# Kernel optimization log

Hardware: AMD Instinct MI355X
Metric: run time of the kernel (lower is better)

Reference implementation:

```python
import jax, jax.numpy as jnp
import numpy as np

N = 50000      # nodes
E = 600000     # edges
IN = 128       # input_dim
HID = 128      # hidden_dim
OUT = 128      # output_dim
H = 4          # heads
D = OUT // H   # head dim
R = 4          # rel_num
L = 2          # n_layer
M = 10000      # len(idx)
EPS = 1e-5


def setup_inputs() -> dict:
    key = jax.random.key(0)
    ks = jax.random.split(key, 16)
    f = jax.random.normal
    inp = {
        "x": f(ks[0], (N, IN), jnp.float32),
        "proj_w": f(ks[1], (IN, HID), jnp.float32) / np.sqrt(IN).astype(np.float32),
        "proj_b": jnp.zeros((HID,), jnp.float32),
        "bn_gamma": jnp.ones((HID,), jnp.float32),
        "bn_beta": jnp.zeros((HID,), jnp.float32),
        # per-layer HGTConv params (stacked on leading L axis; layer0 in=HID, layer1 in=OUT, equal here)
        "q_w": f(ks[2], (L, HID, OUT), jnp.float32) / np.sqrt(HID).astype(np.float32),
        "q_b": jnp.zeros((L, OUT), jnp.float32),
        "k_w": f(ks[3], (L, HID, OUT), jnp.float32) / np.sqrt(HID).astype(np.float32),
        "k_b": jnp.zeros((L, OUT), jnp.float32),
        "v_w": f(ks[4], (L, HID, OUT), jnp.float32) / np.sqrt(HID).astype(np.float32),
        "v_b": jnp.zeros((L, OUT), jnp.float32),
        "a_w": f(ks[5], (L, OUT, OUT), jnp.float32) / np.sqrt(OUT).astype(np.float32),
        "a_b": jnp.zeros((L, OUT), jnp.float32),
        "skip": jnp.ones((L,), jnp.float32),
        "a_rel": f(ks[6], (L, R, H, D, D), jnp.float32) / np.sqrt(D).astype(np.float32),
        "m_rel": f(ks[7], (L, R, H, D, D), jnp.float32) / np.sqrt(D).astype(np.float32),
        "p_rel": jnp.ones((L, R, H), jnp.float32),
        "edge_index": jax.random.randint(ks[8], (2, E), 0, N, dtype=jnp.int32),
        "edge_type": jax.random.randint(ks[9], (E,), 0, R, dtype=jnp.int32),
        "idx": jax.random.randint(ks[10], (M,), 0, N, dtype=jnp.int32),
    }
    return inp


def _hgt_forward(x, proj_w, proj_b, bn_gamma, bn_beta, q_w, q_b, k_w, k_b, v_w, v_b,
                 a_w, a_b, skip, a_rel, m_rel, p_rel, edge_index, edge_type, idx):
    # proj + BatchNorm1d (training-mode batch statistics, biased variance)
    h = x @ proj_w + proj_b
    mu = h.mean(axis=0)
    var = jnp.mean((h - mu) ** 2, axis=0)
    h = (h - mu) * jax.lax.rsqrt(var + EPS) * bn_gamma + bn_beta

    src, dst = edge_index[0], edge_index[1]          # message from src(j) to dst(i)
    seg = dst * R + edge_type                        # per-(dst, relation) softmax segments
    scale = np.float32(1.0 / np.sqrt(D))

    for l in range(L):
        q = (h @ q_w[l] + q_b[l]).reshape(N, H, D)
        k = (h @ k_w[l] + k_b[l]).reshape(N, H, D)
        v = (h @ v_w[l] + v_b[l]).reshape(N, H, D)
        # relation-specific key/value transforms for every node/relation: [N,R,H,D]
        k_all = jnp.einsum('nhd,rhde->nrhe', k, a_rel[l])
        v_all = jnp.einsum('nhd,rhde->nrhe', v, m_rel[l])
        k_e = k_all[src, edge_type]                  # [E,H,D]
        v_e = v_all[src, edge_type]                  # [E,H,D]
        score = jnp.sum(q[dst] * k_e, axis=-1) * p_rel[l][edge_type] * scale  # [E,H]
        # per-relation segment softmax over incoming edges of each dst node
        smax = jax.ops.segment_max(score, seg, num_segments=N * R)
        e = jnp.exp(score - smax[seg])
        denom = jax.ops.segment_sum(e, seg, num_segments=N * R)
        alpha = e / denom[seg]                        # [E,H]
        out = jax.ops.segment_sum(alpha[..., None] * v_e, dst, num_segments=N)
        out = out.reshape(N, OUT)
        out = jax.nn.gelu(out, approximate=False) @ a_w[l] + a_b[l]
        b = jax.nn.sigmoid(skip[l])                   # learned skip gate
        h = b * out + (1.0 - b) * h                   # dims match -> residual mix
    return h[idx]


def reference(x, proj_w, proj_b, bn_gamma, bn_beta, q_w, q_b, k_w, k_b, v_w, v_b,
              a_w, a_b, skip, a_rel, m_rel, p_rel, edge_index, edge_type, idx):
    return _hgt_forward(x, proj_w, proj_b, bn_gamma, bn_beta, q_w, q_b, k_w, k_b,
                        v_w, v_b, a_w, a_b, skip, a_rel, m_rel, p_rel,
                        edge_index, edge_type, idx)
```

## Files before the change

### kernel.cpp

```cpp
#include <hip/hip_runtime.h>
#include <math.h>

#define NN 50000
#define EE 600000
#define MOUT 10000
#define DEGCAP 384
#define NT4 (NN * 4)

typedef short bf16x8 __attribute__((ext_vector_type(8)));
typedef float f32x4 __attribute__((ext_vector_type(4)));

__device__ __forceinline__ unsigned short f2bf(float x) {
    unsigned int u = __float_as_uint(x);
    u = (u + 0x7FFFu + ((u >> 16) & 1u)) >> 16;
    return (unsigned short)u;
}
__device__ __forceinline__ float bf2f(unsigned int b) {
    return __uint_as_float(b << 16);
}

__global__ __launch_bounds__(256) void prep_kernel(
    const float* __restrict__ proj_w, const float* __restrict__ a_w,
    const float* __restrict__ q_w, const float* __restrict__ q_b,
    const float* __restrict__ a_rel,
    const float* __restrict__ k_w, const float* __restrict__ k_b,
    const float* __restrict__ v_w, const float* __restrict__ v_b,
    const float* __restrict__ m_rel, const float* __restrict__ p_rel,
    const float* __restrict__ x,
    unsigned short* __restrict__ wt_pa, unsigned short* __restrict__ qkvw,
    float* __restrict__ fbias, unsigned short* __restrict__ msg_wt,
    unsigned short* __restrict__ x_bf, int* __restrict__ cnt,
    float* __restrict__ stats)
{
    const int b = blockIdx.x, t = threadIdx.x;
    if (b < 192) {
        int wi = b >> 6;
        int flat = (b & 63) * 256 + t;
        int n = flat >> 7, c = flat & 127;
        const float* src = (wi == 0) ? proj_w : (wi == 1) ? a_w : a_w + 16384;
        wt_pa[(size_t)wi * 16384 + n * 128 + c] = f2bf(src[c * 128 + n]);
    } else if (b < 960) {
        int q = b - 192;
        int l = q >= 384 ? 1 : 0;
        int flat = (q - l * 384) * 256 + t;
        int nrow = flat >> 7, c = flat & 127;
        unsigned short* wt = qkvw + (size_t)l * 98304;
        float* fb = fbias + l * 768;
        if (nrow < 512) {
            int r = nrow >> 7, hh = (nrow >> 5) & 3, d = nrow & 31;
            float prl = p_rel[l * 16 + r * 4 + hh] * 0.17677669529663687f;
            const float* qwc = q_w + (size_t)l * 16384 + c * 128 + hh * 32;
            const float* ar  = a_rel + (size_t)(l * 4 + r) * 4096 + hh * 1024 + d * 32;
            float s = 0.f;
            #pragma unroll 8
            for (int e = 0; e < 32; ++e) s += qwc[e] * ar[e];
            wt[(size_t)nrow * 128 + c] = f2bf(s * prl);
            if (c == 0) {
                const float* qb = q_b + l * 128 + hh * 32;
                float bb = 0.f;
                #pragma unroll 8
                for (int e = 0; e < 32; ++e) bb += qb[e] * ar[e];
                fb[nrow] = bb * prl;
            }
        } else {
            int j = nrow - 512;
            int tt = j >> 2, s = j & 3;
            int col = 2 * tt + (s & 1);
            const float* w  = (s < 2) ? k_w : v_w;
            const float* bb = (s < 2) ? k_b : v_b;
            wt[(size_t)nrow * 128 + c] = f2bf(w[(size_t)l * 16384 + c * 128 + col]);
            if (c == 0) fb[nrow] = bb[l * 128 + col];
        }
    } else if (b < 1472) {
        int q = b - 960;
        int l = q >= 256 ? 1 : 0;
        int flat = (q - l * 256) * 256 + t;
        int n = flat >> 9, kk = flat & 511;
        int h = n >> 5, e = n & 31;
        int r = kk >> 7, h2 = (kk >> 5) & 3, d = kk & 31;
        float val = (h2 == h) ? m_rel[(size_t)(l * 4 + r) * 4096 + h * 1024 + d * 32 + e] : 0.f;
        msg_wt[(size_t)l * 65536 + (size_t)n * 512 + kk] = f2bf(val);
    } else if (b < 7722) {
        int i = (b - 1472) * 256 + t;
        if (i < NN * 32) {
            float4 v = ((const float4*)x)[i];
            uint2 pk;
            pk.x = (unsigned int)f2bf(v.x) | ((unsigned int)f2bf(v.y) << 16);
            pk.y = (unsigned int)f2bf(v.z) | ((unsigned int)f2bf(v.w) << 16);
            ((uint2*)x_bf)[i] = pk;
        }
    } else {
        int i = (b - 7722) * 256 + t;
        if (i < NT4) cnt[i] = 0;
        if (i < 256) stats[i] = 0.f;
    }
}

__global__ __launch_bounds__(256) void hist_kernel(const int* __restrict__ ei,
    const int* __restrict__ et, int* __restrict__ cnt, int E)
{
    int e = blockIdx.x * 256 + threadIdx.x;
    if (e < E) atomicAdd(&cnt[ei[E + e] * 4 + et[e]], 1);
}

__global__ __launch_bounds__(256) void scan_block_kernel(const int* __restrict__ cnt,
    int* __restrict__ excl, int* __restrict__ bsum, int n)
{
    __shared__ int tmp[256];
    int i = blockIdx.x * 256 + threadIdx.x;
    int v = (i < n) ? cnt[i] : 0;
    tmp[threadIdx.x] = v;
    __syncthreads();
    for (int ofs = 1; ofs < 256; ofs <<= 1) {
        int t = (threadIdx.x >= ofs) ? tmp[threadIdx.x - ofs] : 0;
        __syncthreads();
        tmp[threadIdx.x] += t;
        __syncthreads();
    }
    if (i < n) excl[i] = tmp[threadIdx.x] - v;
    if (threadIdx.x == 255) bsum[blockIdx.x] = tmp[255];
}

__global__ __launch_bounds__(256) void scan_add_kernel(int* __restrict__ excl,
    const int* __restrict__ bsum, int* __restrict__ fill, int n, int total)
{
    __shared__ int red[256];
    const int b = blockIdx.x;
    int partial = 0;
    for (int j = threadIdx.x; j < b; j += 256) partial += bsum[j];
    red[threadIdx.x] = partial;
    __syncthreads();
    for (int ofs = 128; ofs > 0; ofs >>= 1) {
        if (threadIdx.x < ofs) red[threadIdx.x] += red[threadIdx.x + ofs];
        __syncthreads();
    }
    int prefix = red[0];
    int i = b * 256 + threadIdx.x;
    if (i < n) {
        int o = excl[i] + prefix;
        excl[i] = o;
        fill[i] = o;
    }
    if (b == 0 && threadIdx.x == 0) excl[n] = total;
}

__global__ __launch_bounds__(256) void scatter_kernel(const int* __restrict__ ei,
    const int* __restrict__ et, int* __restrict__ fill, int* __restrict__ pack, int E)
{
    int e = blockIdx.x * 256 + threadIdx.x;
    if (e >= E) return;
    int seg = ei[E + e] * 4 + et[e];
    int p = atomicAdd(&fill[seg], 1);
    pack[p] = ei[e];
}

__global__ __launch_bounds__(256) void projstats_kernel(
    const unsigned short* __restrict__ A, const unsigned short* __restrict__ Wt,
    const float* __restrict__ bias, unsigned short* __restrict__ Cb,
    float* __restrict__ stats, int M)
{
    __shared__ unsigned short As[128 * 40];
    __shared__ unsigned short Bs[128 * 40];
    const int t = threadIdx.x;
    const int wave = t >> 6, lane = t & 63;
    const int quad = lane >> 4, l16 = lane & 15;
    const int row0 = blockIdx.x * 128;
    const int wr = (wave & 1) * 64, wc = (wave >> 1) * 64;
    const int sr = t >> 1, sc = (t & 1) * 16;
    const int grow = row0 + sr;

    f32x4 acc[4][4];
    #pragma unroll
    for (int i = 0; i < 4; ++i)
        #pragma unroll
        for (int j = 0; j < 4; ++j)
            acc[i][j] = (f32x4){0.f, 0.f, 0.f, 0.f};

    uint4 av0 = make_uint4(0,0,0,0), av1 = av0, bv0, bv1;
    if (grow < M) {
        const uint4* ap = (const uint4*)(A + (size_t)grow * 128 + sc);
        av0 = ap[0]; av1 = ap[1];
    }
    {
        const uint4* bp = (const uint4*)(Wt + (size_t)sr * 128 + sc);
        bv0 = bp[0]; bv1 = bp[1];
    }
    for (int it = 0; it < 4; ++it) {
        __syncthreads();
        *(uint4*)(As + sr * 40 + sc)     = av0;
        *(uint4*)(As + sr * 40 + sc + 8) = av1;
        *(uint4*)(Bs + sr * 40 + sc)     = bv0;
        *(uint4*)(Bs + sr * 40 + sc + 8) = bv1;
        __syncthreads();
        if (it + 1 < 4) {
            int kb = (it + 1) * 32;
            if (grow < M) {
                const uint4* ap = (const uint4*)(A + (size_t)grow * 128 + kb + sc);
                av0 = ap[0]; av1 = ap[1];
            }
            const uint4* bp = (const uint4*)(Wt + (size_t)sr * 128 + kb + sc);
            bv0 = bp[0]; bv1 = bp[1];
        }
        bf16x8 af[4], bfr[4];
        #pragma unroll
        for (int f = 0; f < 4; ++f) {
            af[f]  = *(const bf16x8*)(As + (wr + f * 16 + l16) * 40 + quad * 8);
            bfr[f] = *(const bf16x8*)(Bs + (wc + f * 16 + l16) * 40 + quad * 8);
        }
        #pragma unroll
        for (int fr = 0; fr < 4; ++fr)
            #pragma unroll
            for (int fc = 0; fc < 4; ++fc)
                acc[fr][fc] = __builtin_amdgcn_mfma_f32_16x16x32_bf16(
                    af[fr], bfr[fc], acc[fr][fc], 0, 0, 0);
    }

    #pragma unroll
    for (int fc = 0; fc < 4; ++fc) {
        const int col = wc + fc * 16 + l16;
        const float bv = bias[col];
        float s = 0.f, s2 = 0.f;
        #pragma unroll
        for (int fr = 0; fr < 4; ++fr)
            #pragma unroll
            for (int reg = 0; reg < 4; ++reg) {
                int row = row0 + wr + fr * 16 + quad * 4 + reg;
                float val = acc[fr][fc][reg] + bv;
                if (row < M) {
                    Cb[(size_t)row * 128 + col] = f2bf(val);
                    s += val; s2 += val * val;
                }
            }
        s  += __shfl_xor(s, 16);  s  += __shfl_xor(s, 32);
        s2 += __shfl_xor(s2, 16); s2 += __shfl_xor(s2, 32);
        if (quad == 0) {
            atomicAdd(&stats[col], s);
            atomicAdd(&stats[128 + col], s2);
        }
    }
}

__global__ __launch_bounds__(256) void bnqkv_kernel(
    const unsigned short* __restrict__ hb, const float* __restrict__ stats,
    const float* __restrict__ gamma, const float* __restrict__ beta,
    const unsigned short* __restrict__ qkvw, const float* __restrict__ fbias,
    unsigned short* __restrict__ hn, unsigned short* __restrict__ qkv, int M)
{
    __shared__ unsigned short hS[128 * 136];
    __shared__ unsigned short Bs[128 * 40];
    __shared__ float mulS[128], addS[128];
    const int t = threadIdx.x;
    const int row0 = blockIdx.x * 128;
    if (t < 128) {
        float invN = 1.f / 50000.f;
        float mu = stats[t] * invN;
        float var = stats[128 + t] * invN - mu * mu;
        float ml = rsqrtf(var + 1e-5f) * gamma[t];
        mulS[t] = ml;
        addS[t] = beta[t] - mu * ml;
    }
    __syncthreads();
    #pragma unroll
    for (int u = 0; u < 8; ++u) {
        int li = t + u * 256;
        int row = li >> 4, c0 = (li & 15) * 8;
        uint4 pk = make_uint4(0, 0, 0, 0);
        if (row0 + row < M)
            pk = ((const uint4*)(hb + (size_t)(row0 + row) * 128))[li & 15];
        unsigned int w[4] = {pk.x, pk.y, pk.z, pk.w};
        uint4 o;
        unsigned int ov[4];
        #pragma unroll
        for (int g = 0; g < 4; ++g) {
            int c = c0 + g * 2;
            float a0 = bf2f(w[g] & 0xFFFFu) * mulS[c]     + addS[c];
            float a1 = bf2f(w[g] >> 16)     * mulS[c + 1] + addS[c + 1];
            ov[g] = (unsigned int)f2bf(a0) | ((unsigned int)f2bf(a1) << 16);
        }
        o.x = ov[0]; o.y = ov[1]; o.z = ov[2]; o.w = ov[3];
        *(uint4*)(hS + row * 136 + c0) = o;
        if (row0 + row < M)
            ((uint4*)(hn + (size_t)(row0 + row) * 128))[li & 15] = o;
    }
    __syncthreads();

    const int wave = t >> 6, lane = t & 63;
    const int quad = lane >> 4, l16 = lane & 15;
    const int wr = (wave & 1) * 64, wcl = (wave >> 1) * 64;
    const int sr = t >> 1, scc = (t & 1) * 16;
    for (int ch = 0; ch < 6; ++ch) {
        f32x4 acc[4][4];
        #pragma unroll
        for (int i = 0; i < 4; ++i)
            #pragma unroll
            for (int j = 0; j < 4; ++j)
                acc[i][j] = (f32x4){0.f, 0.f, 0.f, 0.f};
        for (int it = 0; it < 4; ++it) {
            __syncthreads();
            const uint4* bp = (const uint4*)(qkvw + (size_t)(ch * 128 + sr) * 128 + it * 32 + scc);
            *(uint4*)(Bs + sr * 40 + scc)     = bp[0];
            *(uint4*)(Bs + sr * 40 + scc + 8) = bp[1];
            __syncthreads();
            bf16x8 af[4], bfr[4];
            #pragma unroll
            for (int f = 0; f < 4; ++f) {
                af[f]  = *(const bf16x8*)(hS + (wr + f * 16 + l16) * 136 + it * 32 + quad * 8);
                bfr[f] = *(const bf16x8*)(Bs + (wcl + f * 16 + l16) * 40 + quad * 8);
            }
            #pragma unroll
            for (int fr = 0; fr < 4; ++fr)
                #pragma unroll
                for (int fc = 0; fc < 4; ++fc)
                    acc[fr][fc] = __builtin_amdgcn_mfma_f32_16x16x32_bf16(
                        af[fr], bfr[fc], acc[fr][fc], 0, 0, 0);
        }
        float b4[4];
        #pragma unroll
        for (int fc = 0; fc < 4; ++fc)
            b4[fc] = fbias[ch * 128 + wcl + fc * 16 + l16];
        #pragma unroll
        for (int fr = 0; fr < 4; ++fr)
            #pragma unroll
            for (int reg = 0; reg < 4; ++reg) {
                int row = row0 + wr + fr * 16 + quad * 4 + reg;
                if (row >= M) continue;
                #pragma unroll
                for (int fc = 0; fc < 4; ++fc) {
                    int col = ch * 128 + wcl + fc * 16 + l16;
                    qkv[(size_t)row * 768 + col] = f2bf(acc[fr][fc][reg] + b4[fc]);
                }
            }
    }
}

__global__ __launch_bounds__(256) void agg_fused_kernel(
    const unsigned short* __restrict__ qkv,
    const int* __restrict__ off4, const int* __restrict__ pack,
    const int* __restrict__ rowmap, unsigned short* __restrict__ aggb, int count)
{
    __shared__ int spack[4][DEGCAP];
    const int wv = threadIdx.x >> 6;
    const int lane = threadIdx.x & 63;
    const int unit = blockIdx.x * 4 + wv;
    if (unit >= count) return;
    const int node = rowmap ? __builtin_amdgcn_readfirstlane(rowmap[unit]) : unit;

    int off_r[5];
    #pragma unroll
    for (int i = 0; i < 5; ++i)
        off_r[i] = __builtin_amdgcn_readfirstlane(off4[node * 4 + i]);
    const int beg = off_r[0];
    const int deg = off_r[4] - beg;
    const bool cached = deg <= DEGCAP;

    const unsigned int* qrow = (const unsigned int*)(qkv + (size_t)node * 768);

    if (cached) {
        for (int i = lane; i < deg; i += 64) spack[wv][i] = pack[beg + i];
        asm volatile("s_waitcnt vmcnt(0) lgkmcnt(0)" ::: "memory");
    }

    unsigned int outw[4];
    for (int r = 0; r < 4; ++r) {
        unsigned int qu = qrow[r * 64 + lane];
        float qx = bf2f(qu & 0xFFFFu);
        float qy = bf2f(qu >> 16);
        float den = 0.f, ax = 0.f, ay = 0.f;

        if (cached) {
            const int rb = off_r[r] - beg, re = off_r[r + 1] - beg;
            for (int i = rb; i < re; i += 4) {
                unsigned int ku[4], vu[4];
                #pragma unroll
                for (int j = 0; j < 4; ++j) {
                    int ii = i + j; if (ii >= re) ii = re - 1;
                    int src = spack[wv][ii];
                    uint2 kv = *(const uint2*)(qkv + (size_t)src * 768 + 512 + lane * 4);
                    ku[j] = kv.x; vu[j] = kv.y;
                }
                float p[4];
                #pragma unroll
                for (int j = 0; j < 4; ++j)
                    p[j] = qx * bf2f(ku[j] & 0xFFFFu) + qy * bf2f(ku[j] >> 16);
                #pragma unroll
                for (int j = 0; j < 4; ++j) {
                    p[j] += __shfl_xor(p[j], 1); p[j] += __shfl_xor(p[j], 2);
                    p[j] += __shfl_xor(p[j], 4); p[j] += __shfl_xor(p[j], 8);
                }
                #pragma unroll
                for (int j = 0; j < 4; ++j) {
                    float s = fminf(fmaxf(p[j], -80.f), 80.f);
                    float e = __expf(s);
                    if (i + j >= re) e = 0.f;
                    den += e;
                    ax += e * bf2f(vu[j] & 0xFFFFu);
                    ay += e * bf2f(vu[j] >> 16);
                }
            }
        } else {
            for (int pp = off_r[r]; pp < off_r[r + 1]; ++pp) {
                int src = __builtin_amdgcn_readfirstlane(pack[pp]);
                uint2 kv = *(const uint2*)(qkv + (size_t)src * 768 + 512 + lane * 4);
                float p0 = qx * bf2f(kv.x & 0xFFFFu) + qy * bf2f(kv.x >> 16);
                p0 += __shfl_xor(p0, 1); p0 += __shfl_xor(p0, 2);
                p0 += __shfl_xor(p0, 4); p0 += __shfl_xor(p0, 8);
                float e = __expf(fminf(fmaxf(p0, -80.f), 80.f));
                den += e;
                ax += e * bf2f(kv.y & 0xFFFFu);
                ay += e * bf2f(kv.y >> 16);
            }
        }
        float inv = den > 0.f ? 1.f / den : 0.f;
        outw[r] = (unsigned int)f2bf(ax * inv) | ((unsigned int)f2bf(ay * inv) << 16);
    }
    unsigned int* op = (unsigned int*)(aggb + (size_t)unit * 512);
    #pragma unroll
    for (int r = 0; r < 4; ++r) op[r * 64 + lane] = outw[r];
}

__global__ __launch_bounds__(256) void mlpqkv_kernel(
    const unsigned short* __restrict__ A, const unsigned short* __restrict__ W3t,
    const unsigned short* __restrict__ AWt, const float* __restrict__ a_bias,
    const float* __restrict__ skipv, const unsigned short* __restrict__ hres,
    const unsigned short* __restrict__ qkvw1, const float* __restrict__ fbias1,
    unsigned short* __restrict__ h1, unsigned short* __restrict__ qkv, int M)
{
    __shared__ unsigned short As[128 * 40];
    __shared__ unsigned short Bs[128 * 40];
    __shared__ unsigned short msgS[128 * 136];
    const int t = threadIdx.x;
    const int wave = t >> 6, lane = t & 63;
    const int quad = lane >> 4, l16 = lane & 15;
    const int row0 = blockIdx.x * 128;
    const int wr = (wave & 1) * 64, wcl = (wave >> 1) * 64;
    const int sr = t >> 1, scc = (t & 1) * 16;
    const int grow = row0 + sr;
    const bool rvalid = grow < M;

    f32x4 acc[4][4];
    #pragma unroll
    for (int i = 0; i < 4; ++i)
        #pragma unroll
        for (int j = 0; j < 4; ++j)
            acc[i][j] = (f32x4){0.f, 0.f, 0.f, 0.f};

    uint4 av0 = make_uint4(0,0,0,0), av1 = av0, bv0, bv1;
    if (rvalid) {
        const uint4* ap = (const uint4*)(A + (size_t)grow * 512 + scc);
        av0 = ap[0]; av1 = ap[1];
    }
    {
        const uint4* bp = (const uint4*)(W3t + (size_t)sr * 512 + scc);
        bv0 = bp[0]; bv1 = bp[1];
    }
    for (int it = 0; it < 16; ++it) {
        __syncthreads();
        *(uint4*)(As + sr * 40 + scc)     = av0;
        *(uint4*)(As + sr * 40 + scc + 8) = av1;
        *(uint4*)(Bs + sr * 40 + scc)     = bv0;
        *(uint4*)(Bs + sr * 40 + scc + 8) = bv1;
        __syncthreads();
        if (it + 1 < 16) {
            int kb = (it + 1) * 32;
            if (rvalid) {
                const uint4* ap = (const uint4*)(A + (size_t)grow * 512 + kb + scc);
                av0 = ap[0]; av1 = ap[1];
            }
            const uint4* bp = (const uint4*)(W3t + (size_t)sr * 512 + kb + scc);
            bv0 = bp[0]; bv1 = bp[1];
        }
        bf16x8 af[4], bfr[4];
        #pragma unroll
        for (int f = 0; f < 4; ++f) {
            af[f]  = *(const bf16x8*)(As + (wr + f * 16 + l16) * 40 + quad * 8);
            bfr[f] = *(const bf16x8*)(Bs + (wcl + f * 16 + l16) * 40 + quad * 8);
        }
        #pragma unroll
        for (int fr = 0; fr < 4; ++fr)
            #pragma unroll
            for (int fc = 0; fc < 4; ++fc)
                acc[fr][fc] = __builtin_amdgcn_mfma_f32_16x16x32_bf16(
                    af[fr], bfr[fc], acc[fr][fc], 0, 0, 0);
    }

    #pragma unroll
    for (int fr = 0; fr < 4; ++fr)
        #pragma unroll
        for (int reg = 0; reg < 4; ++reg) {
            int rl = wr + fr * 16 + quad * 4 + reg;
            #pragma unroll
            for (int fc = 0; fc < 4; ++fc) {
                int col = wcl + fc * 16 + l16;
                float v = acc[fr][fc][reg];
                float gl = 0.5f * v * (1.f + erff(v * 0.70710678118654752f));
                msgS[rl * 136 + col] = f2bf(gl);
            }
        }

    f32x4 acc2[4][4];
    #pragma unroll
    for (int i = 0; i < 4; ++i)
        #pragma unroll
        for (int j = 0; j < 4; ++j)
            acc2[i][j] = (f32x4){0.f, 0.f, 0.f, 0.f};
    for (int it = 0; it < 4; ++it) {
        __syncthreads();
        const uint4* bp = (const uint4*)(AWt + (size_t)sr * 128 + it * 32 + scc);
        *(uint4*)(Bs + sr * 40 + scc)     = bp[0];
        *(uint4*)(Bs + sr * 40 + scc + 8) = bp[1];
        __syncthreads();
        bf16x8 af[4], bfr[4];
        #pragma unroll
        for (int f = 0; f < 4; ++f) {
            af[f]  = *(const bf16x8*)(msgS + (wr + f * 16 + l16) * 136 + it * 32 + quad * 8);
            bfr[f] = *(const bf16x8*)(Bs + (wcl + f * 16 + l16) * 40 + quad * 8);
        }
        #pragma unroll
        for (int fr = 0; fr < 4; ++fr)
            #pragma unroll
            for (int fc = 0; fc < 4; ++fc)
                acc2[fr][fc] = __builtin_amdgcn_mfma_f32_16x16x32_bf16(
                    af[fr], bfr[fc], acc2[fr][fc], 0, 0, 0);
    }

    const float gate = 1.f / (1.f + __expf(-skipv[0]));
    __syncthreads();
    #pragma unroll
    for (int fr = 0; fr < 4; ++fr)
        #pragma unroll
        for (int reg = 0; reg < 4; ++reg) {
            int rl = wr + fr * 16 + quad * 4 + reg;
            int row = row0 + rl;
            #pragma unroll
            for (int fc = 0; fc < 4; ++fc) {
                int col = wcl + fc * 16 + l16;
                float val = acc2[fr][fc][reg] + a_bias[col];
                float nv = val;
                if (row < M) {
                    unsigned int hu = hres[(size_t)row * 128 + col];
                    nv = gate * val + (1.f - gate) * bf2f(hu);
                    h1[(size_t)row * 128 + col] = f2bf(nv);
                }
                msgS[rl * 136 + col] = f2bf(nv);
            }
        }

    for (int ch = 0; ch < 6; ++ch) {
        f32x4 acc3[4][4];
        #pragma unroll
        for (int i = 0; i < 4; ++i)
            #pragma unroll
            for (int j = 0; j < 4; ++j)
                acc3[i][j] = (f32x4){0.f, 0.f, 0.f, 0.f};
        for (int it = 0; it < 4; ++it) {
            __syncthreads();
            const uint4* bp = (const uint4*)(qkvw1 + (size_t)(ch * 128 + sr) * 128 + it * 32 + scc);
            *(uint4*)(Bs + sr * 40 + scc)     = bp[0];
            *(uint4*)(Bs + sr * 40 + scc + 8) = bp[1];
            __syncthreads();
            bf16x8 af[4], bfr[4];
            #pragma unroll
            for (int f = 0; f < 4; ++f) {
                af[f]  = *(const bf16x8*)(msgS + (wr + f * 16 + l16) * 136 + it * 32 + quad * 8);
                bfr[f] = *(const bf16x8*)(Bs + (wcl + f * 16 + l16) * 40 + quad * 8);
            }
            #pragma unroll
            for (int fr = 0; fr < 4; ++fr)
                #pragma unroll
                for (int fc = 0; fc < 4; ++fc)
                    acc3[fr][fc] = __builtin_amdgcn_mfma_f32_16x16x32_bf16(
                        af[fr], bfr[fc], acc3[fr][fc], 0, 0, 0);
        }
        float b4[4];
        #pragma unroll
        for (int fc = 0; fc < 4; ++fc)
            b4[fc] = fbias1[ch * 128 + wcl + fc * 16 + l16];
        #pragma unroll
        for (int fr = 0; fr < 4; ++fr)
            #pragma unroll
            for (int reg = 0; reg < 4; ++reg) {
                int row = row0 + wr + fr * 16 + quad * 4 + reg;
                if (row >= M) continue;
                #pragma unroll
                for (int fc = 0; fc < 4; ++fc) {
                    int col = ch * 128 + wcl + fc * 16 + l16;
                    qkv[(size_t)row * 768 + col] = f2bf(acc3[fr][fc][reg] + b4[fc]);
                }
            }
    }
}

__global__ __launch_bounds__(256) void mlp1_kernel(
    const unsigned short* __restrict__ A, const unsigned short* __restrict__ W3t,
    const unsigned short* __restrict__ AWt, const float* __restrict__ a_bias,
    const float* __restrict__ skipv, const unsigned short* __restrict__ hres,
    const int* __restrict__ rowmap, float* __restrict__ out, int M)
{
    __shared__ unsigned short As[128 * 40];
    __shared__ unsigned short Bs[128 * 40];
    __shared__ unsigned short msgS[128 * 136];
    const int t = threadIdx.x;
    const int wave = t >> 6, lane = t & 63;
    const int quad = lane >> 4, l16 = lane & 15;
    const int row0 = blockIdx.x * 128;
    const int wr = (wave & 1) * 64, wcl = (wave >> 1) * 64;
    const int sr = t >> 1, scc = (t & 1) * 16;
    const int grow = row0 + sr;
    const bool rvalid = grow < M;

    f32x4 acc[4][4];
    #pragma unroll
    for (int i = 0; i < 4; ++i)
        #pragma unroll
        for (int j = 0; j < 4; ++j)
            acc[i][j] = (f32x4){0.f, 0.f, 0.f, 0.f};

    uint4 av0 = make_uint4(0,0,0,0), av1 = av0, bv0, bv1;
    if (rvalid) {
        const uint4* ap = (const uint4*)(A + (size_t)grow * 512 + scc);
        av0 = ap[0]; av1 = ap[1];
    }
    {
        const uint4* bp = (const uint4*)(W3t + (size_t)sr * 512 + scc);
        bv0 = bp[0]; bv1 = bp[1];
    }
    for (int it = 0; it < 16; ++it) {
        __syncthreads();
        *(uint4*)(As + sr * 40 + scc)     = av0;
        *(uint4*)(As + sr * 40 + scc + 8) = av1;
        *(uint4*)(Bs + sr * 40 + scc)     = bv0;
        *(uint4*)(Bs + sr * 40 + scc + 8) = bv1;
        __syncthreads();
        if (it + 1 < 16) {
            int kb = (it + 1) * 32;
            if (rvalid) {
                const uint4* ap = (const uint4*)(A + (size_t)grow * 512 + kb + scc);
                av0 = ap[0]; av1 = ap[1];
            }
            const uint4* bp = (const uint4*)(W3t + (size_t)sr * 512 + kb + scc);
            bv0 = bp[0]; bv1 = bp[1];
        }
        bf16x8 af[4], bfr[4];
        #pragma unroll
        for (int f = 0; f < 4; ++f) {
            af[f]  = *(const bf16x8*)(As + (wr + f * 16 + l16) * 40 + quad * 8);
            bfr[f] = *(const bf16x8*)(Bs + (wcl + f * 16 + l16) * 40 + quad * 8);
        }
        #pragma unroll
        for (int fr = 0; fr < 4; ++fr)
            #pragma unroll
            for (int fc = 0; fc < 4; ++fc)
                acc[fr][fc] = __builtin_amdgcn_mfma_f32_16x16x32_bf16(
                    af[fr], bfr[fc], acc[fr][fc], 0, 0, 0);
    }

    #pragma unroll
    for (int fr = 0; fr < 4; ++fr)
        #pragma unroll
        for (int reg = 0; reg < 4; ++reg) {
            int rl = wr + fr * 16 + quad * 4 + reg;
            #pragma unroll
            for (int fc = 0; fc < 4; ++fc) {
                int col = wcl + fc * 16 + l16;
                float v = acc[fr][fc][reg];
                float gl = 0.5f * v * (1.f + erff(v * 0.70710678118654752f));
                msgS[rl * 136 + col] = f2bf(gl);
            }
        }

    f32x4 acc2[4][4];
    #pragma unroll
    for (int i = 0; i < 4; ++i)
        #pragma unroll
        for (int j = 0; j < 4; ++j)
            acc2[i][j] = (f32x4){0.f, 0.f, 0.f, 0.f};
    for (int it = 0; it < 4; ++it) {
        __syncthreads();
        const uint4* bp = (const uint4*)(AWt + (size_t)sr * 128 + it * 32 + scc);
        *(uint4*)(Bs + sr * 40 + scc)     = bp[0];
        *(uint4*)(Bs + sr * 40 + scc + 8) = bp[1];
        __syncthreads();
        bf16x8 af[4], bfr[4];
        #pragma unroll
        for (int f = 0; f < 4; ++f) {
            af[f]  = *(const bf16x8*)(msgS + (wr + f * 16 + l16) * 136 + it * 32 + quad * 8);
            bfr[f] = *(const bf16x8*)(Bs + (wcl + f * 16 + l16) * 40 + quad * 8);
        }
        #pragma unroll
        for (int fr = 0; fr < 4; ++fr)
            #pragma unroll
            for (int fc = 0; fc < 4; ++fc)
                acc2[fr][fc] = __builtin_amdgcn_mfma_f32_16x16x32_bf16(
                    af[fr], bfr[fc], acc2[fr][fc], 0, 0, 0);
    }

    const float gate = 1.f / (1.f + __expf(-skipv[0]));
    #pragma unroll
    for (int fr = 0; fr < 4; ++fr)
        #pragma unroll
        for (int reg = 0; reg < 4; ++reg) {
            int row = row0 + wr + fr * 16 + quad * 4 + reg;
            if (row >= M) continue;
            int hrow = rowmap[row];
            #pragma unroll
            for (int fc = 0; fc < 4; ++fc) {
                int col = wcl + fc * 16 + l16;
                float val = acc2[fr][fc][reg] + a_bias[col];
                float nv = gate * val + (1.f - gate) * bf2f((unsigned int)hres[(size_t)hrow * 128 + col]);
                out[(size_t)row * 128 + col] = nv;
            }
        }
}

extern "C" void kernel_launch(void* const* d_in, const int* in_sizes, int n_in,
                              void* d_out, int out_size, void* d_ws, size_t ws_size,
                              hipStream_t stream)
{
    const float* x      = (const float*)d_in[0];
    const float* proj_w = (const float*)d_in[1];
    const float* proj_b = (const float*)d_in[2];
    const float* bn_g   = (const float*)d_in[3];
    const float* bn_b   = (const float*)d_in[4];
    const float* q_w    = (const float*)d_in[5];
    const float* q_b    = (const float*)d_in[6];
    const float* k_w    = (const float*)d_in[7];
    const float* k_b    = (const float*)d_in[8];
    const float* v_w    = (const float*)d_in[9];
    const float* v_b    = (const float*)d_in[10];
    const float* a_w    = (const float*)d_in[11];
    const float* a_b    = (const float*)d_in[12];
    const float* skip   = (const float*)d_in[13];
    const float* a_rel  = (const float*)d_in[14];
    const float* m_rel  = (const float*)d_in[15];
    const float* p_rel  = (const float*)d_in[16];
    const int* edge_index = (const int*)d_in[17];
    const int* edge_type  = (const int*)d_in[18];
    const int* idx        = (const int*)d_in[19];
    float* out = (float*)d_out;

    const int N = NN, E = EE;
    float* ws = (float*)d_ws;
    size_t o = 0;
    float* stats  = ws + o;  o += 256;
    float* fbias  = ws + o;  o += 2 * 768;
    int* cnt  = (int*)(ws + o); o += NT4;
    int* off4 = (int*)(ws + o); o += NT4 + 1;
    int* fill = (int*)(ws + o); o += NT4;
    int* bsum = (int*)(ws + o); o += 1024;
    int* pack = (int*)(ws + o); o += E;
    unsigned short* x_bf   = (unsigned short*)(ws + o); o += (size_t)N * 64;
    unsigned short* h_bf   = (unsigned short*)(ws + o); o += (size_t)N * 64;
    unsigned short* hn_bf  = (unsigned short*)(ws + o); o += (size_t)N * 64;
    unsigned short* h1_bf  = (unsigned short*)(ws + o); o += (size_t)N * 64;
    unsigned short* qkv_bf = (unsigned short*)(ws + o); o += (size_t)N * 384;
    unsigned short* agg_bf = (unsigned short*)(ws + o); o += (size_t)N * 256;
    unsigned short* wt_pa  = (unsigned short*)(ws + o); o += 3 * 16384 / 2;
    unsigned short* qkvw   = (unsigned short*)(ws + o); o += 2 * 98304 / 2;
    unsigned short* msg_wt = (unsigned short*)(ws + o); o += 2 * 65536 / 2;

    const int NB4 = (NT4 + 255) / 256;
    const int g = (N + 127) / 128;

    prep_kernel<<<7722 + NB4, 256, 0, stream>>>(
        proj_w, a_w, q_w, q_b, a_rel, k_w, k_b, v_w, v_b, m_rel, p_rel, x,
        wt_pa, qkvw, fbias, msg_wt, x_bf, cnt, stats);

    hist_kernel<<<(E + 255) / 256, 256, 0, stream>>>(edge_index, edge_type, cnt, E);
    scan_block_kernel<<<NB4, 256, 0, stream>>>(cnt, off4, bsum, NT4);
    scan_add_kernel<<<NB4, 256, 0, stream>>>(off4, bsum, fill, NT4, E);
    scatter_kernel<<<(E + 255) / 256, 256, 0, stream>>>(edge_index, edge_type, fill, pack, E);

    projstats_kernel<<<g, 256, 0, stream>>>(x_bf, wt_pa, proj_b, h_bf, stats, N);

    bnqkv_kernel<<<g, 256, 0, stream>>>(h_bf, stats, bn_g, bn_b, qkvw, fbias,
                                        hn_bf, qkv_bf, N);

    agg_fused_kernel<<<(N + 3) / 4, 256, 0, stream>>>(qkv_bf, off4, pack, nullptr,
                                                      agg_bf, N);

    mlpqkv_kernel<<<g, 256, 0, stream>>>(agg_bf, msg_wt, wt_pa + 16384, a_b, skip,
                                         hn_bf, qkvw + 98304, fbias + 768,
                                         h1_bf, qkv_bf, N);

    agg_fused_kernel<<<(MOUT + 3) / 4, 256, 0, stream>>>(qkv_bf, off4, pack, idx,
                                                         agg_bf, MOUT);

    mlp1_kernel<<<(MOUT + 127) / 128, 256, 0, stream>>>(agg_bf, msg_wt + 65536,
                                                        wt_pa + 2 * 16384, a_b + 128,
                                                        skip + 1, h1_bf, idx, out, MOUT);
}
```

Baseline: 441.9 us.

## Compute layer-1 queries only for output nodes and skip unused h1 writes

The layer-0 MLP kernel now produces only the key/message chunks (chunks 4-5) of the layer-1 projection for all nodes. A new q1_kernel gathers h1 rows for the output indices and computes their queries separately, and the second aggregation reads q from that compact buffer. A node mask built during CSR scatter limits h1 stores to nodes that appear in idx. This removes the query GEMM and most h1 writes for the full graph, at the cost of an extra small kernel, a byte mask, and reuse of the cnt and x_bf workspace buffers.

```diff
diff --git a/kernel.cpp b/kernel.cpp
--- a/kernel.cpp
+++ b/kernel.cpp
@@ -122,7 +122,8 @@
 }
 
 __global__ __launch_bounds__(256) void scan_add_kernel(int* __restrict__ excl,
-    const int* __restrict__ bsum, int* __restrict__ fill, int n, int total)
+    const int* __restrict__ bsum, int* __restrict__ fill,
+    int* __restrict__ maskz, int n, int total)
 {
     __shared__ int red[256];
     const int b = blockIdx.x;
@@ -141,17 +142,20 @@
         excl[i] = o;
         fill[i] = o;
     }
+    if (i < 12500) maskz[i] = 0;
     if (b == 0 && threadIdx.x == 0) excl[n] = total;
 }
 
 __global__ __launch_bounds__(256) void scatter_kernel(const int* __restrict__ ei,
-    const int* __restrict__ et, int* __restrict__ fill, int* __restrict__ pack, int E)
+    const int* __restrict__ et, int* __restrict__ fill, int* __restrict__ pack,
+    const int* __restrict__ idxp, unsigned char* __restrict__ mask, int Mo, int E)
 {
     int e = blockIdx.x * 256 + threadIdx.x;
     if (e >= E) return;
     int seg = ei[E + e] * 4 + et[e];
     int p = atomicAdd(&fill[seg], 1);
     pack[p] = ei[e];
+    if (e < Mo) mask[idxp[e]] = 1;
 }
 
 __global__ __launch_bounds__(256) void projstats_kernel(
@@ -335,6 +339,7 @@
 
 __global__ __launch_bounds__(256) void agg_fused_kernel(
     const unsigned short* __restrict__ qkv,
+    const unsigned short* __restrict__ qbuf, int qpitch,
     const int* __restrict__ off4, const int* __restrict__ pack,
     const int* __restrict__ rowmap, unsigned short* __restrict__ aggb, int count)
 {
@@ -353,7 +358,7 @@
     const int deg = off_r[4] - beg;
     const bool cached = deg <= DEGCAP;
 
-    const unsigned int* qrow = (const unsigned int*)(qkv + (size_t)node * 768);
+    const unsigned int* qrow = (const unsigned int*)(qbuf + (size_t)unit * qpitch);
 
     if (cached) {
         for (int i = lane; i < deg; i += 64) spack[wv][i] = pack[beg + i];
@@ -423,6 +428,7 @@
     const unsigned short* __restrict__ AWt, const float* __restrict__ a_bias,
     const float* __restrict__ skipv, const unsigned short* __restrict__ hres,
     const unsigned short* __restrict__ qkvw1, const float* __restrict__ fbias1,
+    const unsigned char* __restrict__ mask,
     unsigned short* __restrict__ h1, unsigned short* __restrict__ qkv, int M)
 {
     __shared__ unsigned short As[128 * 40];
@@ -531,21 +537,23 @@
         for (int reg = 0; reg < 4; ++reg) {
             int rl = wr + fr * 16 + quad * 4 + reg;
             int row = row0 + rl;
+            const bool rv = row < M;
+            const bool mw = rv && mask[row];
             #pragma unroll
             for (int fc = 0; fc < 4; ++fc) {
                 int col = wcl + fc * 16 + l16;
                 float val = acc2[fr][fc][reg] + a_bias[col];
                 float nv = val;
-                if (row < M) {
+                if (rv) {
                     unsigned int hu = hres[(size_t)row * 128 + col];
                     nv = gate * val + (1.f - gate) * bf2f(hu);
-                    h1[(size_t)row * 128 + col] = f2bf(nv);
+                    if (mw) h1[(size_t)row * 128 + col] = f2bf(nv);
                 }
                 msgS[rl * 136 + col] = f2bf(nv);
             }
         }
 
-    for (int ch = 0; ch < 6; ++ch) {
+    for (int ch = 4; ch < 6; ++ch) {
         f32x4 acc3[4][4];
         #pragma unroll
         for (int i = 0; i < 4; ++i)
@@ -585,6 +593,77 @@
                 for (int fc = 0; fc < 4; ++fc) {
                     int col = ch * 128 + wcl + fc * 16 + l16;
                     qkv[(size_t)row * 768 + col] = f2bf(acc3[fr][fc][reg] + b4[fc]);
+                }
+            }
+    }
+}
+
+__global__ __launch_bounds__(256) void q1_kernel(
+    const unsigned short* __restrict__ h1, const int* __restrict__ idxp,
+    const unsigned short* __restrict__ qkvw1, const float* __restrict__ fbias1,
+    unsigned short* __restrict__ q1, int M)
+{
+    __shared__ unsigned short hS[128 * 136];
+    __shared__ unsigned short Bs[128 * 40];
+    const int t = threadIdx.x;
+    const int row0 = blockIdx.x * 128;
+    #pragma unroll
+    for (int u = 0; u < 8; ++u) {
+        int li = t + u * 256;
+        int row = li >> 4, c = li & 15;
+        uint4 pk = make_uint4(0, 0, 0, 0);
+        if (row0 + row < M) {
+            int node = idxp[row0 + row];
+            pk = ((const uint4*)(h1 + (size_t)node * 128))[c];
+        }
+        *(uint4*)(hS + row * 136 + c * 8) = pk;
+    }
+    __syncthreads();
+
+    const int wave = t >> 6, lane = t & 63;
+    const int quad = lane >> 4, l16 = lane & 15;
+    const int wr = (wave & 1) * 64, wcl = (wave >> 1) * 64;
+    const int sr = t >> 1, scc = (t & 1) * 16;
+    for (int ch = 0; ch < 4; ++ch) {
+        f32x4 acc[4][4];
+        #pragma unroll
+        for (int i = 0; i < 4; ++i)
+            #pragma unroll
+            for (int j = 0; j < 4; ++j)
+                acc[i][j] = (f32x4){0.f, 0.f, 0.f, 0.f};
+        for (int it = 0; it < 4; ++it) {
+            __syncthreads();
+            const uint4* bp = (const uint4*)(qkvw1 + (size_t)(ch * 128 + sr) * 128 + it * 32 + scc);
+            *(uint4*)(Bs + sr * 40 + scc)     = bp[0];
+            *(uint4*)(Bs + sr * 40 + scc + 8) = bp[1];
+            __syncthreads();
+            bf16x8 af[4], bfr[4];
+            #pragma unroll
+            for (int f = 0; f < 4; ++f) {
+                af[f]  = *(const bf16x8*)(hS + (wr + f * 16 + l16) * 136 + it * 32 + quad * 8);
+                bfr[f] = *(const bf16x8*)(Bs + (wcl + f * 16 + l16) * 40 + quad * 8);
+            }
+            #pragma unroll
+            for (int fr = 0; fr < 4; ++fr)
+                #pragma unroll
+                for (int fc = 0; fc < 4; ++fc)
+                    acc[fr][fc] = __builtin_amdgcn_mfma_f32_16x16x32_bf16(
+                        af[fr], bfr[fc], acc[fr][fc], 0, 0, 0);
+        }
+        float b4[4];
+        #pragma unroll
+        for (int fc = 0; fc < 4; ++fc)
+            b4[fc] = fbias1[ch * 128 + wcl + fc * 16 + l16];
+        #pragma unroll
+        for (int fr = 0; fr < 4; ++fr)
+            #pragma unroll
+            for (int reg = 0; reg < 4; ++reg) {
+                int row = row0 + wr + fr * 16 + quad * 4 + reg;
+                if (row >= M) continue;
+                #pragma unroll
+                for (int fc = 0; fc < 4; ++fc) {
+                    int col = ch * 128 + wcl + fc * 16 + l16;
+                    q1[(size_t)row * 512 + col] = f2bf(acc[fr][fc][reg] + b4[fc]);
                 }
             }
     }
@@ -758,6 +837,9 @@
     unsigned short* qkvw   = (unsigned short*)(ws + o); o += 2 * 98304 / 2;
     unsigned short* msg_wt = (unsigned short*)(ws + o); o += 2 * 65536 / 2;
 
+    unsigned char* mask = (unsigned char*)cnt;
+    unsigned short* q1 = x_bf;
+
     const int NB4 = (NT4 + 255) / 256;
     const int g = (N + 127) / 128;
 
@@ -767,23 +849,27 @@
 
     hist_kernel<<<(E + 255) / 256, 256, 0, stream>>>(edge_index, edge_type, cnt, E);
     scan_block_kernel<<<NB4, 256, 0, stream>>>(cnt, off4, bsum, NT4);
-    scan_add_kernel<<<NB4, 256, 0, stream>>>(off4, bsum, fill, NT4, E);
-    scatter_kernel<<<(E + 255) / 256, 256, 0, stream>>>(edge_index, edge_type, fill, pack, E);
+    scan_add_kernel<<<NB4, 256, 0, stream>>>(off4, bsum, fill, cnt, NT4, E);
+    scatter_kernel<<<(E + 255) / 256, 256, 0, stream>>>(edge_index, edge_type, fill,
+                                                        pack, idx, mask, MOUT, E);
 
     projstats_kernel<<<g, 256, 0, stream>>>(x_bf, wt_pa, proj_b, h_bf, stats, N);
 
     bnqkv_kernel<<<g, 256, 0, stream>>>(h_bf, stats, bn_g, bn_b, qkvw, fbias,
                                         hn_bf, qkv_bf, N);
 
-    agg_fused_kernel<<<(N + 3) / 4, 256, 0, stream>>>(qkv_bf, off4, pack, nullptr,
-                                                      agg_bf, N);
+    agg_fused_kernel<<<(N + 3) / 4, 256, 0, stream>>>(qkv_bf, qkv_bf, 768,
+                                                      off4, pack, nullptr, agg_bf, N);
 
     mlpqkv_kernel<<<g, 256, 0, stream>>>(agg_bf, msg_wt, wt_pa + 16384, a_b, skip,
                                          hn_bf, qkvw + 98304, fbias + 768,
-                                         h1_bf, qkv_bf, N);
-
-    agg_fused_kernel<<<(MOUT + 3) / 4, 256, 0, stream>>>(qkv_bf, off4, pack, idx,
-                                                         agg_bf, MOUT);
+                                         mask, h1_bf, qkv_bf, N);
+
+    q1_kernel<<<(MOUT + 127) / 128, 256, 0, stream>>>(h1_bf, idx, qkvw + 98304,
+                                                      fbias + 768, q1, MOUT);
+
+    agg_fused_kernel<<<(MOUT + 3) / 4, 256, 0, stream>>>(qkv_bf, q1, 512,
+                                                         off4, pack, idx, agg_bf, MOUT);
 
     mlp1_kernel<<<(MOUT + 127) / 128, 256, 0, stream>>>(agg_bf, msg_wt + 65536,
                                                         wt_pa + 2 * 16384, a_b + 128,
```

Result: slower. 454.9 us (+3.0%).
